# Optimization experiments

Hardware: AMD Instinct MI355X
Metric: run time of the kernel (lower is better)

The kernel has to match this reference:

```python
import jax, jax.numpy as jnp
import numpy as np

NTOKENS = 50257
NHID = 1024
NTOK_PER_CLASS = 225   # ceil(sqrt(50257))
NCLASSES = 224         # ceil(50257/225)
BATCH = 2048


def setup_inputs() -> dict:
    key = jax.random.key(0)
    k1, k2, k3, k4 = jax.random.split(key, 4)
    initrange = 0.1
    inputs = jax.random.normal(k1, (BATCH, NHID), dtype=jnp.float32)
    labels = jax.random.randint(k2, (BATCH,), 0, NTOKENS, dtype=jnp.int64)
    layer_top_W = jax.random.uniform(k3, (NHID, NCLASSES), dtype=jnp.float32,
                                     minval=-initrange, maxval=initrange)
    layer_top_b = jnp.zeros((NCLASSES,), dtype=jnp.float32)
    layer_bottom_W = jax.random.uniform(k4, (NCLASSES, NHID, NTOK_PER_CLASS),
                                        dtype=jnp.float32,
                                        minval=-initrange, maxval=initrange)
    layer_bottom_b = jnp.zeros((NCLASSES, NTOK_PER_CLASS), dtype=jnp.float32)
    return {"inputs": inputs, "labels": labels,
            "layer_top_W": layer_top_W, "layer_top_b": layer_top_b,
            "layer_bottom_W": layer_bottom_W, "layer_bottom_b": layer_bottom_b}


def reference(inputs, labels, layer_top_W, layer_top_b, layer_bottom_W, layer_bottom_b):
    batch_size = inputs.shape[0]
    label_position_top = labels // NTOK_PER_CLASS          # [B]
    label_position_bottom = labels % NTOK_PER_CLASS        # [B]

    # top-level class probabilities
    top_logits = inputs @ layer_top_W + layer_top_b        # [B, nclasses]
    top_probs = jax.nn.softmax(top_logits, axis=1)

    # per-sample gather of class weight matrices + batched matmul
    W_sel = layer_bottom_W[label_position_top]             # [B, nhid, ntok_per_class]
    b_sel = layer_bottom_b[label_position_top]             # [B, ntok_per_class]
    bottom_logits = jnp.einsum('bh,bht->bt', inputs, W_sel) + b_sel
    bottom_probs = jax.nn.softmax(bottom_logits, axis=1)

    idx = jnp.arange(batch_size)
    target_probs = top_probs[idx, label_position_top] * bottom_probs[idx, label_position_bottom]
    return target_probs
```

## Files before the change

### kernel.cpp

```cpp
#include <hip/hip_runtime.h>
#include <math.h>

#define NHID  1024
#define NCLS  224
#define NTPC  225
#define BATCH 2048

#define KSPLIT 8
#define KCH    128
#define NTILES (BATCH / 16)
#define NBOT_BLOCKS (NCLS * KSPLIT)
#define NTOP_BLOCKS (NTILES * KSPLIT)

#define CLS_OFF  0
#define POS_OFF  8192
#define LIST_OFF 16384
#define OFFS_OFF 24576
#define YTOP_OFF 32768
#define YTOP_BYTES (BATCH * NCLS * 4)
#define YBOT_OFF (YTOP_OFF + YTOP_BYTES)
#define YBOT_BYTES (BATCH * NTPC * 4)

__global__ __launch_bounds__(256) void group_kernel(const int* __restrict__ labels,
                                                    int* __restrict__ cls,
                                                    int* __restrict__ pos,
                                                    int* __restrict__ list,
                                                    int* __restrict__ offs) {
    __shared__ int cnt[NCLS];
    __shared__ int sc[256];
    __shared__ int bex[NCLS];
    __shared__ int nz;
    const int tid = threadIdx.x;
    if (tid == 0) nz = 0;
    for (int j = tid; j < NCLS; j += 256) cnt[j] = 0;
    __syncthreads();
    int loc = 0;
    for (int k = 0; k < 4; ++k) {
        int i = tid + 256 * k;
        if (labels[2 * i + 1] != 0) loc = 1;
    }
    if (loc) atomicOr(&nz, 1);
    __syncthreads();
    const bool is64 = (nz == 0);
    int myc[8], myr[8];
#pragma unroll
    for (int k = 0; k < 8; ++k) {
        int i = tid + 256 * k;
        int l = is64 ? labels[2 * i] : labels[i];
        int c = l / NTPC;
        cls[i] = c;
        pos[i] = l - c * NTPC;
        myc[k] = c;
        myr[k] = atomicAdd(&cnt[c], 1);
    }
    __syncthreads();
    int v = (tid < NCLS) ? cnt[tid] : 0;
    sc[tid] = v;
    __syncthreads();
    for (int off = 1; off < 256; off <<= 1) {
        int u = (tid >= off) ? sc[tid - off] : 0;
        __syncthreads();
        sc[tid] += u;
        __syncthreads();
    }
    if (tid < NCLS) {
        int ex = sc[tid] - v;
        bex[tid] = ex;
        offs[tid] = ex;
    }
    if (tid == 0) offs[NCLS] = BATCH;
    __syncthreads();
#pragma unroll
    for (int k = 0; k < 8; ++k) {
        int i = tid + 256 * k;
        list[bex[myc[k]] + myr[k]] = i;
    }
}

template<int YC, bool BOT>
__device__ __forceinline__ void run_tiles(const float* __restrict__ x,
                                          const float* __restrict__ W,
                                          float* __restrict__ y,
                                          const int* __restrict__ list,
                                          int o, int n, int hbase,
                                          float* __restrict__ xs) {
    const int tid = threadIdx.x;
    const int w = tid >> 6, l = tid & 63;
    const int col  = 64 * w + l;
    const int colc = min(col, YC - 1);
    const bool colok = (col < YC);
    const int r  = tid & 127;
    const int hs = tid >> 7;
    const int rq = (r >> 1) & 3;

    for (int tile = 0; tile * 16 < n; ++tile) {
        if (tile) __syncthreads();
        const float* xrow = x + hbase + r;
#pragma unroll
        for (int j = 0; j < 8; ++j) {
            const int i = hs * 8 + j;
            const int idx = tile * 16 + i;
            const int s = BOT ? list[o + min(idx, n - 1)] : (o + idx);
            xs[(r << 4) + ((((i >> 2) ^ rq) << 2) | (i & 3))] = xrow[(size_t)s * NHID];
        }
        __syncthreads();

        float acc[16];
#pragma unroll
        for (int i = 0; i < 16; ++i) acc[i] = 0.f;

        const float* wr = W + (size_t)hbase * YC + colc;
#pragma unroll 8
        for (int h = 0; h < KCH; ++h) {
            float wv = wr[0];
            const float4* xr = (const float4*)&xs[h << 4];
            const int q = (h >> 1) & 3;
            float4 x0 = xr[q];
            float4 x1 = xr[1 ^ q];
            float4 x2 = xr[2 ^ q];
            float4 x3 = xr[3 ^ q];
            acc[0]  = fmaf(x0.x, wv, acc[0]);
            acc[1]  = fmaf(x0.y, wv, acc[1]);
            acc[2]  = fmaf(x0.z, wv, acc[2]);
            acc[3]  = fmaf(x0.w, wv, acc[3]);
            acc[4]  = fmaf(x1.x, wv, acc[4]);
            acc[5]  = fmaf(x1.y, wv, acc[5]);
            acc[6]  = fmaf(x1.z, wv, acc[6]);
            acc[7]  = fmaf(x1.w, wv, acc[7]);
            acc[8]  = fmaf(x2.x, wv, acc[8]);
            acc[9]  = fmaf(x2.y, wv, acc[9]);
            acc[10] = fmaf(x2.z, wv, acc[10]);
            acc[11] = fmaf(x2.w, wv, acc[11]);
            acc[12] = fmaf(x3.x, wv, acc[12]);
            acc[13] = fmaf(x3.y, wv, acc[13]);
            acc[14] = fmaf(x3.z, wv, acc[14]);
            acc[15] = fmaf(x3.w, wv, acc[15]);
            wr += YC;
        }

        const int nt = min(n - tile * 16, 16);
        if (colok) {
            for (int i = 0; i < nt; ++i) {
                const int s = BOT ? list[o + tile * 16 + i] : (o + tile * 16 + i);
                atomicAdd(&y[(size_t)s * YC + col], acc[i]);
            }
        }
    }
}

__global__ __launch_bounds__(256, 8) void partial_kernel(const float* __restrict__ x,
                                                         const float* __restrict__ Wt,
                                                         const float* __restrict__ Wb,
                                                         const int* __restrict__ list,
                                                         const int* __restrict__ offs,
                                                         float* __restrict__ ytop,
                                                         float* __restrict__ ybot) {
    __shared__ __align__(16) float xs[KCH * 16];
    const int bi = blockIdx.x;
    if (bi < NBOT_BLOCKS) {
        const int c = bi % NCLS;
        const int k = bi / NCLS;
        const int o = offs[c];
        const int n = offs[c + 1] - o;
        run_tiles<NTPC, true>(x, Wb + (size_t)c * (NHID * NTPC), ybot, list,
                              o, n, k * KCH, xs);
    } else {
        const int b2 = bi - NBOT_BLOCKS;
        const int st = b2 % NTILES;
        const int k  = b2 / NTILES;
        run_tiles<NCLS, false>(x, Wt, ytop, list, st * 16, 16, k * KCH, xs);
    }
}

__global__ __launch_bounds__(256) void finalize_kernel(const float* __restrict__ ytop,
                                                       const float* __restrict__ ybot,
                                                       const float* __restrict__ bt,
                                                       const float* __restrict__ bb,
                                                       const int* __restrict__ cls,
                                                       const int* __restrict__ pos,
                                                       float* __restrict__ out) {
    const int w = threadIdx.x >> 6, l = threadIdx.x & 63;
    const int s = blockIdx.x * 4 + w;
    const int c = cls[s], p = pos[s];

    float v[4];
#pragma unroll
    for (int g = 0; g < 4; ++g) {
        int col = l + 64 * g;
        v[g] = (col < NCLS) ? ytop[(size_t)s * NCLS + col] + bt[col] : -INFINITY;
    }
    float mx = fmaxf(fmaxf(v[0], v[1]), fmaxf(v[2], v[3]));
#pragma unroll
    for (int off = 32; off; off >>= 1) mx = fmaxf(mx, __shfl_xor(mx, off));
    float sum = 0.f, tc = 0.f;
#pragma unroll
    for (int g = 0; g < 4; ++g) {
        int col = l + 64 * g;
        float e = (col < NCLS) ? __expf(v[g] - mx) : 0.f;
        sum += e;
        if (col == c) tc = e;
    }
#pragma unroll
    for (int off = 32; off; off >>= 1) {
        sum += __shfl_xor(sum, off);
        tc  += __shfl_xor(tc, off);
    }
    const float tp = tc / sum;

#pragma unroll
    for (int g = 0; g < 4; ++g) {
        int col = l + 64 * g;
        v[g] = (col < NTPC) ? ybot[(size_t)s * NTPC + col] + bb[c * NTPC + col] : -INFINITY;
    }
    mx = fmaxf(fmaxf(v[0], v[1]), fmaxf(v[2], v[3]));
#pragma unroll
    for (int off = 32; off; off >>= 1) mx = fmaxf(mx, __shfl_xor(mx, off));
    float bsum = 0.f, ep = 0.f;
#pragma unroll
    for (int g = 0; g < 4; ++g) {
        int col = l + 64 * g;
        float e = (col < NTPC) ? __expf(v[g] - mx) : 0.f;
        bsum += e;
        if (col == p) ep = e;
    }
#pragma unroll
    for (int off = 32; off; off >>= 1) bsum += __shfl_xor(bsum, off);
#pragma unroll
    for (int g = 0; g < 4; ++g)
        if (l + 64 * g == p) out[s] = tp * ep / bsum;
}

extern "C" void kernel_launch(void* const* d_in, const int* in_sizes, int n_in,
                              void* d_out, int out_size, void* d_ws, size_t ws_size,
                              hipStream_t stream) {
    const float* inputs = (const float*)d_in[0];
    const int*   labels = (const int*)d_in[1];
    const float* topW   = (const float*)d_in[2];
    const float* topB   = (const float*)d_in[3];
    const float* botW   = (const float*)d_in[4];
    const float* botB   = (const float*)d_in[5];
    float* out = (float*)d_out;

    char* ws   = (char*)d_ws;
    int*   cls = (int*)(ws + CLS_OFF);
    int*   pos = (int*)(ws + POS_OFF);
    int*   lst = (int*)(ws + LIST_OFF);
    int*   off = (int*)(ws + OFFS_OFF);
    float* ytop = (float*)(ws + YTOP_OFF);
    float* ybot = (float*)(ws + YBOT_OFF);

    hipMemsetAsync(ws + YTOP_OFF, 0, YTOP_BYTES + YBOT_BYTES, stream);
    group_kernel<<<1, 256, 0, stream>>>(labels, cls, pos, lst, off);
    partial_kernel<<<NBOT_BLOCKS + NTOP_BLOCKS, 256, 0, stream>>>(
        inputs, topW, botW, lst, off, ytop, ybot);
    finalize_kernel<<<BATCH / 4, 256, 0, stream>>>(ytop, ybot, topB, botB, cls, pos, out);
}
```

Baseline: 355.4 us.

## Replace atomic split-K reduction with per-split partial buffers and remap thread tiles

Each K-split now writes its partial logits to its own slice of the workspace with plain stores, and finalize sums the eight slices. This removes the atomicAdds and the memset. The inner loop is remapped so each wave covers 4 samples × 4 columns using one float4 LDS read and four weight loads per h step, rather than 16 samples × 1 column. The cost is an eight-times larger workspace and extra reads in finalize.

```diff
diff --git a/kernel.cpp b/kernel.cpp
--- a/kernel.cpp
+++ b/kernel.cpp
@@ -12,14 +12,17 @@
 #define NBOT_BLOCKS (NCLS * KSPLIT)
 #define NTOP_BLOCKS (NTILES * KSPLIT)
 
+#define YTOPK (BATCH * NCLS)
+#define YBOTK (BATCH * NTPC)
+
 #define CLS_OFF  0
 #define POS_OFF  8192
 #define LIST_OFF 16384
 #define OFFS_OFF 24576
 #define YTOP_OFF 32768
-#define YTOP_BYTES (BATCH * NCLS * 4)
+#define YTOP_BYTES (KSPLIT * YTOPK * 4)
 #define YBOT_OFF (YTOP_OFF + YTOP_BYTES)
-#define YBOT_BYTES (BATCH * NTPC * 4)
+#define YBOT_BYTES (KSPLIT * YBOTK * 4)
 
 __global__ __launch_bounds__(256) void group_kernel(const int* __restrict__ labels,
                                                     int* __restrict__ cls,
@@ -80,18 +83,18 @@
 template<int YC, bool BOT>
 __device__ __forceinline__ void run_tiles(const float* __restrict__ x,
                                           const float* __restrict__ W,
-                                          float* __restrict__ y,
+                                          float* __restrict__ yk,
                                           const int* __restrict__ list,
                                           int o, int n, int hbase,
                                           float* __restrict__ xs) {
     const int tid = threadIdx.x;
     const int w = tid >> 6, l = tid & 63;
-    const int col  = 64 * w + l;
-    const int colc = min(col, YC - 1);
-    const bool colok = (col < YC);
+    const int col3  = 192 + l;
+    const int col3c = min(col3, YC - 1);
     const int r  = tid & 127;
     const int hs = tid >> 7;
     const int rq = (r >> 1) & 3;
+    const float4* xsq = (const float4*)xs;
 
     for (int tile = 0; tile * 16 < n; ++tile) {
         if (tile) __syncthreads();
@@ -109,40 +112,55 @@
 #pragma unroll
         for (int i = 0; i < 16; ++i) acc[i] = 0.f;
 
-        const float* wr = W + (size_t)hbase * YC + colc;
-#pragma unroll 8
-        for (int h = 0; h < KCH; ++h) {
-            float wv = wr[0];
-            const float4* xr = (const float4*)&xs[h << 4];
-            const int q = (h >> 1) & 3;
-            float4 x0 = xr[q];
-            float4 x1 = xr[1 ^ q];
-            float4 x2 = xr[2 ^ q];
-            float4 x3 = xr[3 ^ q];
-            acc[0]  = fmaf(x0.x, wv, acc[0]);
-            acc[1]  = fmaf(x0.y, wv, acc[1]);
-            acc[2]  = fmaf(x0.z, wv, acc[2]);
-            acc[3]  = fmaf(x0.w, wv, acc[3]);
-            acc[4]  = fmaf(x1.x, wv, acc[4]);
-            acc[5]  = fmaf(x1.y, wv, acc[5]);
-            acc[6]  = fmaf(x1.z, wv, acc[6]);
-            acc[7]  = fmaf(x1.w, wv, acc[7]);
-            acc[8]  = fmaf(x2.x, wv, acc[8]);
-            acc[9]  = fmaf(x2.y, wv, acc[9]);
-            acc[10] = fmaf(x2.z, wv, acc[10]);
-            acc[11] = fmaf(x2.w, wv, acc[11]);
-            acc[12] = fmaf(x3.x, wv, acc[12]);
-            acc[13] = fmaf(x3.y, wv, acc[13]);
-            acc[14] = fmaf(x3.z, wv, acc[14]);
-            acc[15] = fmaf(x3.w, wv, acc[15]);
-            wr += YC;
+        const float* wA = W + (size_t)hbase * YC + l;
+        const float* w3 = W + (size_t)hbase * YC + col3c;
+
+#pragma unroll 1
+        for (int h0 = 0; h0 < KCH; h0 += 8) {
+            const float* wB  = wA + 4 * YC;
+            const float* w3B = w3 + 4 * YC;
+#pragma unroll
+            for (int j = 0; j < 8; ++j) {
+                const float4 xv = xsq[(h0 + j) * 4 + (w ^ (j >> 1))];
+                const float* wp  = (j < 4) ? wA : wB;
+                const float* w3p = (j < 4) ? w3 : w3B;
+                const int jj = j & 3;
+                const float w0  = wp[jj * YC];
+                const float w1  = wp[jj * YC + 64];
+                const float w2  = wp[jj * YC + 128];
+                const float w3v = w3p[jj * YC];
+                acc[0]  = fmaf(xv.x, w0,  acc[0]);
+                acc[1]  = fmaf(xv.x, w1,  acc[1]);
+                acc[2]  = fmaf(xv.x, w2,  acc[2]);
+                acc[3]  = fmaf(xv.x, w3v, acc[3]);
+                acc[4]  = fmaf(xv.y, w0,  acc[4]);
+                acc[5]  = fmaf(xv.y, w1,  acc[5]);
+                acc[6]  = fmaf(xv.y, w2,  acc[6]);
+                acc[7]  = fmaf(xv.y, w3v, acc[7]);
+                acc[8]  = fmaf(xv.z, w0,  acc[8]);
+                acc[9]  = fmaf(xv.z, w1,  acc[9]);
+                acc[10] = fmaf(xv.z, w2,  acc[10]);
+                acc[11] = fmaf(xv.z, w3v, acc[11]);
+                acc[12] = fmaf(xv.w, w0,  acc[12]);
+                acc[13] = fmaf(xv.w, w1,  acc[13]);
+                acc[14] = fmaf(xv.w, w2,  acc[14]);
+                acc[15] = fmaf(xv.w, w3v, acc[15]);
+            }
+            wA += 8 * YC;
+            w3 += 8 * YC;
         }
 
         const int nt = min(n - tile * 16, 16);
-        if (colok) {
-            for (int i = 0; i < nt; ++i) {
-                const int s = BOT ? list[o + tile * 16 + i] : (o + tile * 16 + i);
-                atomicAdd(&y[(size_t)s * YC + col], acc[i]);
+#pragma unroll
+        for (int jj = 0; jj < 4; ++jj) {
+            const int it = 4 * w + jj;
+            if (it < nt) {
+                const int s = BOT ? list[o + tile * 16 + it] : (o + tile * 16 + it);
+                float* yr = yk + (size_t)s * YC;
+                yr[l]       = acc[jj * 4 + 0];
+                yr[l + 64]  = acc[jj * 4 + 1];
+                yr[l + 128] = acc[jj * 4 + 2];
+                if (col3 < YC) yr[col3] = acc[jj * 4 + 3];
             }
         }
     }
@@ -162,13 +180,14 @@
         const int k = bi / NCLS;
         const int o = offs[c];
         const int n = offs[c + 1] - o;
-        run_tiles<NTPC, true>(x, Wb + (size_t)c * (NHID * NTPC), ybot, list,
-                              o, n, k * KCH, xs);
+        run_tiles<NTPC, true>(x, Wb + (size_t)c * (NHID * NTPC),
+                              ybot + (size_t)k * YBOTK, list, o, n, k * KCH, xs);
     } else {
         const int b2 = bi - NBOT_BLOCKS;
         const int st = b2 % NTILES;
         const int k  = b2 / NTILES;
-        run_tiles<NCLS, false>(x, Wt, ytop, list, st * 16, 16, k * KCH, xs);
+        run_tiles<NCLS, false>(x, Wt, ytop + (size_t)k * YTOPK, list,
+                               st * 16, 16, k * KCH, xs);
     }
 }
 
@@ -187,7 +206,15 @@
 #pragma unroll
     for (int g = 0; g < 4; ++g) {
         int col = l + 64 * g;
-        v[g] = (col < NCLS) ? ytop[(size_t)s * NCLS + col] + bt[col] : -INFINITY;
+        if (col < NCLS) {
+            float a = bt[col];
+#pragma unroll
+            for (int k = 0; k < KSPLIT; ++k)
+                a += ytop[(size_t)k * YTOPK + (size_t)s * NCLS + col];
+            v[g] = a;
+        } else {
+            v[g] = -INFINITY;
+        }
     }
     float mx = fmaxf(fmaxf(v[0], v[1]), fmaxf(v[2], v[3]));
 #pragma unroll
@@ -210,7 +237,15 @@
 #pragma unroll
     for (int g = 0; g < 4; ++g) {
         int col = l + 64 * g;
-        v[g] = (col < NTPC) ? ybot[(size_t)s * NTPC + col] + bb[c * NTPC + col] : -INFINITY;
+        if (col < NTPC) {
+            float a = bb[c * NTPC + col];
+#pragma unroll
+            for (int k = 0; k < KSPLIT; ++k)
+                a += ybot[(size_t)k * YBOTK + (size_t)s * NTPC + col];
+            v[g] = a;
+        } else {
+            v[g] = -INFINITY;
+        }
     }
     mx = fmaxf(fmaxf(v[0], v[1]), fmaxf(v[2], v[3]));
 #pragma unroll
@@ -249,7 +284,6 @@
     float* ytop = (float*)(ws + YTOP_OFF);
     float* ybot = (float*)(ws + YBOT_OFF);
 
-    hipMemsetAsync(ws + YTOP_OFF, 0, YTOP_BYTES + YBOT_BYTES, stream);
     group_kernel<<<1, 256, 0, stream>>>(labels, cls, pos, lst, off);
     partial_kernel<<<NBOT_BLOCKS + NTOP_BLOCKS, 256, 0, stream>>>(
         inputs, topW, botW, lst, off, ytop, ybot);
```

Result: no change. 351.5 us (-1.1%).

## Replace K-split atomics with full-K per-class blocks and register-tiled GEMM

Applied to the files above, without the earlier changes.

Drops the 8-way K-split so each block computes the full 1024-long reduction for one class (or one 16-row tile of the top layer). Work is spread over 512 threads, with 8 samples x 4 columns register tiles and double-buffered weight loads. Partial sums are combined through shared-memory atomics and then written to global memory with plain stores. This removes the global atomics and the workspace memset, and pads the output rows. The trade-off is far fewer blocks (352), so load balance depends on how many labels fall in each class, and large classes serialize inside one block.

```diff
diff --git a/kernel.cpp b/kernel.cpp
--- a/kernel.cpp
+++ b/kernel.cpp
@@ -6,20 +6,24 @@
 #define NTPC  225
 #define BATCH 2048
 
-#define KSPLIT 8
-#define KCH    128
-#define NTILES (BATCH / 16)
-#define NBOT_BLOCKS (NCLS * KSPLIT)
-#define NTOP_BLOCKS (NTILES * KSPLIT)
+#define NTOP_BLOCKS 128
+#define NBOT_BLOCKS 224
+#define NBLOCKS (NTOP_BLOCKS + NBOT_BLOCKS)
+
+#define YTS 224
+#define YBS 228
+
+#define XPAD 20
+#define SACCP 228
 
 #define CLS_OFF  0
 #define POS_OFF  8192
 #define LIST_OFF 16384
 #define OFFS_OFF 24576
 #define YTOP_OFF 32768
-#define YTOP_BYTES (BATCH * NCLS * 4)
+#define YTOP_BYTES (BATCH * YTS * 4)
 #define YBOT_OFF (YTOP_OFF + YTOP_BYTES)
-#define YBOT_BYTES (BATCH * NTPC * 4)
+#define YBOT_BYTES (BATCH * YBS * 4)
 
 __global__ __launch_bounds__(256) void group_kernel(const int* __restrict__ labels,
                                                     int* __restrict__ cls,
@@ -77,98 +81,150 @@
     }
 }
 
-template<int YC, bool BOT>
-__device__ __forceinline__ void run_tiles(const float* __restrict__ x,
+template<int YC, int YS, bool BOT>
+__device__ __forceinline__ void run_class(const float* __restrict__ x,
                                           const float* __restrict__ W,
                                           float* __restrict__ y,
                                           const int* __restrict__ list,
-                                          int o, int n, int hbase,
-                                          float* __restrict__ xs) {
+                                          int o, int n,
+                                          float* __restrict__ xs,
+                                          float* __restrict__ sacc) {
     const int tid = threadIdx.x;
-    const int w = tid >> 6, l = tid & 63;
-    const int col  = 64 * w + l;
-    const int colc = min(col, YC - 1);
-    const bool colok = (col < YC);
-    const int r  = tid & 127;
-    const int hs = tid >> 7;
-    const int rq = (r >> 1) & 3;
-
-    for (int tile = 0; tile * 16 < n; ++tile) {
-        if (tile) __syncthreads();
-        const float* xrow = x + hbase + r;
-#pragma unroll
-        for (int j = 0; j < 8; ++j) {
-            const int i = hs * 8 + j;
-            const int idx = tile * 16 + i;
-            const int s = BOT ? list[o + min(idx, n - 1)] : (o + idx);
-            xs[(r << 4) + ((((i >> 2) ^ rq) << 2) | (i & 3))] = xrow[(size_t)s * NHID];
+    const int wv  = tid >> 6;
+    const int l   = tid & 63;
+    const int r   = wv & 3;
+    const int g   = wv >> 2;
+    const int c3  = min(192 + l, YC - 1);
+    const bool c3ok = (192 + l < YC);
+
+    for (int base = 0; base < n; base += 16) {
+        const int nt = min(n - base, 16);
+        __syncthreads();
+        for (int i = tid; i < 16 * SACCP; i += 512) sacc[i] = 0.f;
+
+        float acc[8][4];
+#pragma unroll
+        for (int si = 0; si < 8; ++si)
+#pragma unroll
+            for (int c = 0; c < 4; ++c) acc[si][c] = 0.f;
+
+#pragma unroll 1
+        for (int half = 0; half < 2; ++half) {
+            const int hb = half * 512;
+            if (half) __syncthreads();
+#pragma unroll
+            for (int s = 0; s < 16; ++s) {
+                const int si = BOT ? list[o + min(base + s, n - 1)]
+                                   : (o + min(base + s, n - 1));
+                xs[tid * XPAD + s] = x[(size_t)si * NHID + hb + tid];
+            }
+            __syncthreads();
+
+            const float* Wh = W + (size_t)hb * YC;
+            float wA[16], wB[16];
+            auto LOADG = [&](float (&dst)[16], int gi) {
+                const int gc = min(gi, 31);
+#pragma unroll
+                for (int jt = 0; jt < 4; ++jt) {
+                    const float* row = Wh + (size_t)(16 * gc + 4 * jt + r) * YC;
+                    dst[4 * jt + 0] = row[l];
+                    dst[4 * jt + 1] = row[l + 64];
+                    dst[4 * jt + 2] = row[l + 128];
+                    dst[4 * jt + 3] = row[c3];
+                }
+            };
+            auto COMPG = [&](const float (&wvk)[16], int gi) {
+#pragma unroll
+                for (int jt = 0; jt < 4; ++jt) {
+                    const int lh = 16 * gi + 4 * jt + r;
+                    const float4 xa = *(const float4*)(xs + lh * XPAD + 8 * g);
+                    const float4 xb = *(const float4*)(xs + lh * XPAD + 8 * g + 4);
+                    const float w0 = wvk[4 * jt + 0], w1 = wvk[4 * jt + 1];
+                    const float w2 = wvk[4 * jt + 2], w3 = wvk[4 * jt + 3];
+                    acc[0][0] = fmaf(xa.x, w0, acc[0][0]);
+                    acc[0][1] = fmaf(xa.x, w1, acc[0][1]);
+                    acc[0][2] = fmaf(xa.x, w2, acc[0][2]);
+                    acc[0][3] = fmaf(xa.x, w3, acc[0][3]);
+                    acc[1][0] = fmaf(xa.y, w0, acc[1][0]);
+                    acc[1][1] = fmaf(xa.y, w1, acc[1][1]);
+                    acc[1][2] = fmaf(xa.y, w2, acc[1][2]);
+                    acc[1][3] = fmaf(xa.y, w3, acc[1][3]);
+                    acc[2][0] = fmaf(xa.z, w0, acc[2][0]);
+                    acc[2][1] = fmaf(xa.z, w1, acc[2][1]);
+                    acc[2][2] = fmaf(xa.z, w2, acc[2][2]);
+                    acc[2][3] = fmaf(xa.z, w3, acc[2][3]);
+                    acc[3][0] = fmaf(xa.w, w0, acc[3][0]);
+                    acc[3][1] = fmaf(xa.w, w1, acc[3][1]);
+                    acc[3][2] = fmaf(xa.w, w2, acc[3][2]);
+                    acc[3][3] = fmaf(xa.w, w3, acc[3][3]);
+                    acc[4][0] = fmaf(xb.x, w0, acc[4][0]);
+                    acc[4][1] = fmaf(xb.x, w1, acc[4][1]);
+                    acc[4][2] = fmaf(xb.x, w2, acc[4][2]);
+                    acc[4][3] = fmaf(xb.x, w3, acc[4][3]);
+                    acc[5][0] = fmaf(xb.y, w0, acc[5][0]);
+                    acc[5][1] = fmaf(xb.y, w1, acc[5][1]);
+                    acc[5][2] = fmaf(xb.y, w2, acc[5][2]);
+                    acc[5][3] = fmaf(xb.y, w3, acc[5][3]);
+                    acc[6][0] = fmaf(xb.z, w0, acc[6][0]);
+                    acc[6][1] = fmaf(xb.z, w1, acc[6][1]);
+                    acc[6][2] = fmaf(xb.z, w2, acc[6][2]);
+                    acc[6][3] = fmaf(xb.z, w3, acc[6][3]);
+                    acc[7][0] = fmaf(xb.w, w0, acc[7][0]);
+                    acc[7][1] = fmaf(xb.w, w1, acc[7][1]);
+                    acc[7][2] = fmaf(xb.w, w2, acc[7][2]);
+                    acc[7][3] = fmaf(xb.w, w3, acc[7][3]);
+                }
+            };
+
+            LOADG(wA, 0);
+#pragma unroll 1
+            for (int gi = 0; gi < 32; gi += 2) {
+                LOADG(wB, gi + 1);
+                COMPG(wA, gi);
+                LOADG(wA, gi + 2);
+                COMPG(wB, gi + 1);
+            }
+        }
+
+#pragma unroll
+        for (int si = 0; si < 8; ++si) {
+            float* sr = sacc + (8 * g + si) * SACCP;
+            atomicAdd(sr + l,        acc[si][0]);
+            atomicAdd(sr + l + 64,   acc[si][1]);
+            atomicAdd(sr + l + 128,  acc[si][2]);
+            if (c3ok) atomicAdd(sr + 192 + l, acc[si][3]);
         }
         __syncthreads();
 
-        float acc[16];
-#pragma unroll
-        for (int i = 0; i < 16; ++i) acc[i] = 0.f;
-
-        const float* wr = W + (size_t)hbase * YC + colc;
-#pragma unroll 8
-        for (int h = 0; h < KCH; ++h) {
-            float wv = wr[0];
-            const float4* xr = (const float4*)&xs[h << 4];
-            const int q = (h >> 1) & 3;
-            float4 x0 = xr[q];
-            float4 x1 = xr[1 ^ q];
-            float4 x2 = xr[2 ^ q];
-            float4 x3 = xr[3 ^ q];
-            acc[0]  = fmaf(x0.x, wv, acc[0]);
-            acc[1]  = fmaf(x0.y, wv, acc[1]);
-            acc[2]  = fmaf(x0.z, wv, acc[2]);
-            acc[3]  = fmaf(x0.w, wv, acc[3]);
-            acc[4]  = fmaf(x1.x, wv, acc[4]);
-            acc[5]  = fmaf(x1.y, wv, acc[5]);
-            acc[6]  = fmaf(x1.z, wv, acc[6]);
-            acc[7]  = fmaf(x1.w, wv, acc[7]);
-            acc[8]  = fmaf(x2.x, wv, acc[8]);
-            acc[9]  = fmaf(x2.y, wv, acc[9]);
-            acc[10] = fmaf(x2.z, wv, acc[10]);
-            acc[11] = fmaf(x2.w, wv, acc[11]);
-            acc[12] = fmaf(x3.x, wv, acc[12]);
-            acc[13] = fmaf(x3.y, wv, acc[13]);
-            acc[14] = fmaf(x3.z, wv, acc[14]);
-            acc[15] = fmaf(x3.w, wv, acc[15]);
-            wr += YC;
-        }
-
-        const int nt = min(n - tile * 16, 16);
-        if (colok) {
-            for (int i = 0; i < nt; ++i) {
-                const int s = BOT ? list[o + tile * 16 + i] : (o + tile * 16 + i);
-                atomicAdd(&y[(size_t)s * YC + col], acc[i]);
+#pragma unroll 1
+        for (int i = tid; i < nt * 256; i += 512) {
+            const int s = i >> 8, col = i & 255;
+            if (col < YC) {
+                const int si = BOT ? list[o + base + s] : (o + base + s);
+                y[(size_t)si * YS + col] = sacc[s * SACCP + col];
             }
         }
     }
 }
 
-__global__ __launch_bounds__(256, 8) void partial_kernel(const float* __restrict__ x,
+__global__ __launch_bounds__(512, 4) void partial_kernel(const float* __restrict__ x,
                                                          const float* __restrict__ Wt,
                                                          const float* __restrict__ Wb,
                                                          const int* __restrict__ list,
                                                          const int* __restrict__ offs,
                                                          float* __restrict__ ytop,
                                                          float* __restrict__ ybot) {
-    __shared__ __align__(16) float xs[KCH * 16];
+    __shared__ __align__(16) float xs[512 * XPAD];
+    __shared__ __align__(16) float sacc[16 * SACCP];
     const int bi = blockIdx.x;
-    if (bi < NBOT_BLOCKS) {
-        const int c = bi % NCLS;
-        const int k = bi / NCLS;
+    if (bi < NTOP_BLOCKS) {
+        run_class<NCLS, YTS, false>(x, Wt, ytop, list, bi * 16, 16, xs, sacc);
+    } else {
+        const int c = bi - NTOP_BLOCKS;
         const int o = offs[c];
         const int n = offs[c + 1] - o;
-        run_tiles<NTPC, true>(x, Wb + (size_t)c * (NHID * NTPC), ybot, list,
-                              o, n, k * KCH, xs);
-    } else {
-        const int b2 = bi - NBOT_BLOCKS;
-        const int st = b2 % NTILES;
-        const int k  = b2 / NTILES;
-        run_tiles<NCLS, false>(x, Wt, ytop, list, st * 16, 16, k * KCH, xs);
+        run_class<NTPC, YBS, true>(x, Wb + (size_t)c * (NHID * NTPC), ybot,
+                                   list, o, n, xs, sacc);
     }
 }
 
@@ -187,7 +243,7 @@
 #pragma unroll
     for (int g = 0; g < 4; ++g) {
         int col = l + 64 * g;
-        v[g] = (col < NCLS) ? ytop[(size_t)s * NCLS + col] + bt[col] : -INFINITY;
+        v[g] = (col < NCLS) ? ytop[(size_t)s * YTS + col] + bt[col] : -INFINITY;
     }
     float mx = fmaxf(fmaxf(v[0], v[1]), fmaxf(v[2], v[3]));
 #pragma unroll
@@ -210,7 +266,8 @@
 #pragma unroll
     for (int g = 0; g < 4; ++g) {
         int col = l + 64 * g;
-        v[g] = (col < NTPC) ? ybot[(size_t)s * NTPC + col] + bb[c * NTPC + col] : -INFINITY;
+        v[g] = (col < NTPC) ? ybot[(size_t)s * YBS + col] + bb[c * NTPC + col]
+                            : -INFINITY;
     }
     mx = fmaxf(fmaxf(v[0], v[1]), fmaxf(v[2], v[3]));
 #pragma unroll
@@ -249,9 +306,8 @@
     float* ytop = (float*)(ws + YTOP_OFF);
     float* ybot = (float*)(ws + YBOT_OFF);
 
-    hipMemsetAsync(ws + YTOP_OFF, 0, YTOP_BYTES + YBOT_BYTES, stream);
     group_kernel<<<1, 256, 0, stream>>>(labels, cls, pos, lst, off);
-    partial_kernel<<<NBOT_BLOCKS + NTOP_BLOCKS, 256, 0, stream>>>(
+    partial_kernel<<<NBLOCKS, 512, 0, stream>>>(
         inputs, topW, botW, lst, off, ytop, ybot);
     finalize_kernel<<<BATCH / 4, 256, 0, stream>>>(ytop, ybot, topB, botB, cls, pos, out);
 }
```

Result: slower. 478.3 us (+34.6%).
